# Kernel optimization log

Measured on AMD Instinct MI355X. Metric: run time of the kernel, lower is better.

Reference implementation:

```python
import jax, jax.numpy as jnp
import numpy as np
from jax import lax

LUT_SIZE = 33
BACKBONE_SIZE = 256
N_BASIS = 3


def _identity_lut(size):
    coords = jnp.linspace(0.0, 1.0, size)
    r, g, b = jnp.meshgrid(coords, coords, coords, indexing='ij')
    return jnp.stack([r.ravel(), g.ravel(), b.ravel()], axis=-1)  # [size^3, 3]


def setup_inputs() -> dict:
    key = jax.random.key(0)
    k_img, k_lut, k1, k2, kd = jax.random.split(key, 5)
    B, H, W = 4, 1080, 1920
    image = jax.random.uniform(k_img, (B, 3, H, W), dtype=jnp.float32)
    ident = _identity_lut(LUT_SIZE)  # [35937, 3]
    basis_luts = ident[None].repeat(N_BASIS, axis=0) + 0.05 * jax.random.normal(k_lut, (N_BASIS, LUT_SIZE ** 3, 3), dtype=jnp.float32)
    conv1_w = jax.random.normal(k1, (16, 3, 3, 3), dtype=jnp.float32) * 0.1
    conv1_b = jnp.zeros((16,), jnp.float32)
    conv2_w = jax.random.normal(k2, (32, 16, 3, 3), dtype=jnp.float32) * 0.1
    conv2_b = jnp.zeros((32,), jnp.float32)
    dense_w = jax.random.normal(kd, (32, 3), dtype=jnp.float32) * 0.1
    dense_b = jnp.zeros((3,), jnp.float32)
    return {"image": image, "basis_luts": basis_luts, "conv1_w": conv1_w, "conv1_b": conv1_b,
            "conv2_w": conv2_w, "conv2_b": conv2_b, "dense_w": dense_w, "dense_b": dense_b}


def _backbone(thumb, conv1_w, conv1_b, conv2_w, conv2_b, dense_w, dense_b):
    # Lightweight CNN -> softmax weights over basis LUTs. [B,3,256,256] -> [B,n_basis]
    x = lax.conv_general_dilated(thumb, conv1_w, (2, 2), 'SAME') + conv1_b[None, :, None, None]
    x = jax.nn.relu(x)
    x = lax.conv_general_dilated(x, conv2_w, (2, 2), 'SAME') + conv2_b[None, :, None, None]
    x = jax.nn.relu(x)
    x = x.mean(axis=(2, 3))  # global average pool -> [B, 32]
    return jax.nn.softmax(x @ dense_w + dense_b, axis=-1)


def _apply_lut(image, lut):
    # image [B,3,H,W] in [0,1]; lut [B,S,S,S,3] laid out as (r,g,b) grid axes.
    # Replicates F.grid_sample(mode='bilinear', padding_mode='border', align_corners=True)
    # on a 5D volume where grid x-coord = R channel -> LUT's b-axis (last grid axis),
    # y = G -> g-axis, z = B -> r-axis (exactly the axis mapping of the torch code).
    B, C, H, W = image.shape
    S = lut.shape[1]
    px = image.transpose(0, 2, 3, 1).reshape(B, H * W, 3)  # [B,P,3] = (R,G,B)
    pos = jnp.clip(px, 0.0, 1.0) * (S - 1)  # align_corners=True + border clamp
    i0 = jnp.clip(jnp.floor(pos).astype(jnp.int32), 0, S - 2)
    f = pos - i0.astype(pos.dtype)
    i1 = i0 + 1
    # axis mapping: z (LUT axis 0) <- channel 2 (Blue); y (axis 1) <- G; x (axis 2) <- R
    z0, y0, x0 = i0[..., 2], i0[..., 1], i0[..., 0]
    z1, y1, x1 = i1[..., 2], i1[..., 1], i1[..., 0]
    fz, fy, fx = f[..., 2], f[..., 1], f[..., 0]
    lut_flat = lut.reshape(B, S * S * S, 3)

    def gather(z, y, x):
        idx = (z * S + y) * S + x  # [B,P]
        return jnp.take_along_axis(lut_flat, idx[..., None], axis=1)  # [B,P,3]

    wz0, wz1 = (1.0 - fz)[..., None], fz[..., None]
    wy0, wy1 = (1.0 - fy)[..., None], fy[..., None]
    wx0, wx1 = (1.0 - fx)[..., None], fx[..., None]
    out = (wz0 * (wy0 * (wx0 * gather(z0, y0, x0) + wx1 * gather(z0, y0, x1))
                  + wy1 * (wx0 * gather(z0, y1, x0) + wx1 * gather(z0, y1, x1)))
           + wz1 * (wy0 * (wx0 * gather(z1, y0, x0) + wx1 * gather(z1, y0, x1))
                    + wy1 * (wx0 * gather(z1, y1, x0) + wx1 * gather(z1, y1, x1))))
    out = out.reshape(B, H, W, 3).transpose(0, 3, 1, 2)
    return jnp.clip(out, 0.0, 1.0)


def reference(image, basis_luts, conv1_w, conv1_b, conv2_w, conv2_b, dense_w, dense_b):
    B = image.shape[0]
    S = LUT_SIZE
    thumb = jax.image.resize(image, (B, 3, BACKBONE_SIZE, BACKBONE_SIZE), method='linear')
    weights = _backbone(thumb, conv1_w, conv1_b, conv2_w, conv2_b, dense_w, dense_b)  # [B,n]
    blended = jnp.einsum('bn,npc->bpc', weights, basis_luts)  # [B, S^3, 3]
    lut = blended.reshape(B, S, S, S, 3)
    return _apply_lut(image, lut)
```

## Files before the change

kernel.cpp:

```cpp
#include <hip/hip_runtime.h>
#include <hip/hip_bf16.h>
#include <hip/hip_fp16.h>

#define LUT_S 33
#define LUT_P (LUT_S*LUT_S*LUT_S)
#define CELLS 32768
#define IMG_H 1080
#define IMG_W 1920
#define TH 256
#define TW 256

__global__ __launch_bounds__(256)
void resize_w_kernel(const float* __restrict__ img, float* __restrict__ tmp) {
    __shared__ float srow[IMG_W];
    int r = blockIdx.x;
    const float4* row4 = (const float4*)(img + (size_t)r * IMG_W);
    float4* s4 = (float4*)srow;
    for (int i = threadIdx.x; i < IMG_W / 4; i += 256) s4[i] = row4[i];
    __syncthreads();
    int ow = threadIdx.x;
    const float kscale = 7.5f;
    float sf = (ow + 0.5f) * 7.5f - 0.5f;
    int lo = (int)ceilf(sf - kscale); if (lo < 0) lo = 0;
    int hi = (int)floorf(sf + kscale); if (hi > IMG_W - 1) hi = IMG_W - 1;
    float acc = 0.f, wsum = 0.f;
    for (int i = lo; i <= hi; ++i) {
        float w = 1.0f - fabsf(sf - (float)i) * (1.0f / 7.5f);
        if (w > 0.f) { acc += w * srow[i]; wsum += w; }
    }
    tmp[(size_t)r * TW + ow] = acc / wsum;
}

__global__ void resize_h_kernel(const float* __restrict__ tmp,
                                float* __restrict__ thumb, int total) {
    int e = blockIdx.x * blockDim.x + threadIdx.x;
    if (e >= total) return;
    int ow = e & 255;
    int oh = (e >> 8) & 255;
    int pl = e >> 16;
    const float kscale = 4.21875f;
    float sf = (oh + 0.5f) * 4.21875f - 0.5f;
    int lo = (int)ceilf(sf - kscale); if (lo < 0) lo = 0;
    int hi = (int)floorf(sf + kscale); if (hi > IMG_H - 1) hi = IMG_H - 1;
    const float* col = tmp + (size_t)pl * IMG_H * TW + ow;
    float acc = 0.f, wsum = 0.f;
    for (int i = lo; i <= hi; ++i) {
        float w = 1.0f - fabsf(sf - (float)i) * (1.0f / 4.21875f);
        if (w > 0.f) { acc += w * col[(size_t)i * TW]; wsum += w; }
    }
    thumb[e] = acc / wsum;
}

__global__ void conv1_kernel(const float* __restrict__ thumb,
                             const float* __restrict__ w,
                             const float* __restrict__ bias,
                             float* __restrict__ out, int total) {
    int e = blockIdx.x * blockDim.x + threadIdx.x;
    if (e >= total) return;
    int ow = e & 127;
    int oh = (e >> 7) & 127;
    int b  = e >> 14;
    float acc[16];
    #pragma unroll
    for (int oc = 0; oc < 16; ++oc) acc[oc] = bias[oc];
    for (int ic = 0; ic < 3; ++ic) {
        const float* tp = thumb + ((size_t)(b * 3 + ic) * 256) * 256;
        #pragma unroll
        for (int kh = 0; kh < 3; ++kh) {
            int ih = oh * 2 + kh;
            if (ih >= 256) continue;
            #pragma unroll
            for (int kw = 0; kw < 3; ++kw) {
                int iw = ow * 2 + kw;
                if (iw >= 256) continue;
                float v = tp[ih * 256 + iw];
                #pragma unroll
                for (int oc = 0; oc < 16; ++oc)
                    acc[oc] += v * w[(oc * 3 + ic) * 9 + kh * 3 + kw];
            }
        }
    }
    size_t o = ((size_t)b * 16 << 14) + (oh << 7) + ow;
    #pragma unroll
    for (int oc = 0; oc < 16; ++oc)
        out[o + ((size_t)oc << 14)] = fmaxf(acc[oc], 0.f);
}

__global__ void conv2_pool_kernel(const float* __restrict__ c1,
                                  const float* __restrict__ w,
                                  const float* __restrict__ bias,
                                  float* __restrict__ partial, int total) {
    int e = blockIdx.x * blockDim.x + threadIdx.x;
    if (e >= total) return;
    int sp = e & 4095;
    int g  = (e >> 12) & 3;
    int b  = e >> 14;
    int ow = sp & 63, oh = sp >> 6;
    float acc[8];
    #pragma unroll
    for (int j = 0; j < 8; ++j) acc[j] = bias[g * 8 + j];
    for (int ic = 0; ic < 16; ++ic) {
        const float* ip = c1 + ((size_t)(b * 16 + ic) << 14);
        #pragma unroll
        for (int kh = 0; kh < 3; ++kh) {
            int ih = oh * 2 + kh;
            if (ih >= 128) continue;
            #pragma unroll
            for (int kw = 0; kw < 3; ++kw) {
                int iw = ow * 2 + kw;
                if (iw >= 128) continue;
                float v = ip[(ih << 7) + iw];
                #pragma unroll
                for (int j = 0; j < 8; ++j)
                    acc[j] += v * w[((g * 8 + j) * 16 + ic) * 9 + kh * 3 + kw];
            }
        }
    }
    #pragma unroll
    for (int j = 0; j < 8; ++j) {
        float val = fmaxf(acc[j], 0.f);
        #pragma unroll
        for (int off = 32; off > 0; off >>= 1) val += __shfl_down(val, off, 64);
        acc[j] = val;
    }
    if ((threadIdx.x & 63) == 0) {
        #pragma unroll
        for (int j = 0; j < 8; ++j)
            partial[((b * 32 + g * 8 + j) << 6) + oh] = acc[j];
    }
}

__global__ void head_kernel(const float* __restrict__ partial,
                            const float* __restrict__ dw,
                            const float* __restrict__ db,
                            float* __restrict__ wts, int B) {
    __shared__ float sp[8 * 32];
    __shared__ float lg[8 * 3];
    int t = threadIdx.x;
    if (t < B * 32) {
        const float4* p4 = (const float4*)(partial + (t << 6));
        float s = 0.f;
        #pragma unroll
        for (int i = 0; i < 16; ++i) {
            float4 v = p4[i];
            s += v.x + v.y + v.z + v.w;
        }
        sp[t] = s * (1.0f / 4096.0f);
    }
    __syncthreads();
    if (t < B * 3) {
        int b = t / 3, n = t - b * 3;
        float acc = db[n];
        for (int ch = 0; ch < 32; ++ch) acc += sp[b * 32 + ch] * dw[ch * 3 + n];
        lg[t] = acc;
    }
    __syncthreads();
    if (t < B) {
        float a = lg[t * 3 + 0], bb = lg[t * 3 + 1], c = lg[t * 3 + 2];
        float m = fmaxf(a, fmaxf(bb, c));
        float e0 = expf(a - m), e1 = expf(bb - m), e2 = expf(c - m);
        float inv = 1.0f / (e0 + e1 + e2);
        wts[t * 3 + 0] = e0 * inv;
        wts[t * 3 + 1] = e1 * inv;
        wts[t * 3 + 2] = e2 * inv;
    }
}

__global__ void blend_cells_kernel(const float* __restrict__ basis,
                                   const float* __restrict__ wts,
                                   uint4* __restrict__ cells, int total) {
    int e = blockIdx.x * blockDim.x + threadIdx.x;
    if (e >= total) return;
    int b    = e >> 15;
    int cidx = e & (CELLS - 1);
    int cx = cidx & 31, cy = (cidx >> 5) & 31, cz = cidx >> 10;
    float w0 = wts[b * 3 + 0], w1 = wts[b * 3 + 1], w2 = wts[b * 3 + 2];
    const float* b0 = basis;
    const float* b1 = basis + (size_t)LUT_P * 3;
    const float* b2 = basis + (size_t)2 * LUT_P * 3;
    float v[24];
    float mn = 1e30f, mx = -1e30f;
    #pragma unroll
    for (int c = 0; c < 8; ++c) {
        int dx = c & 1, dy = (c >> 1) & 1, dz = c >> 2;
        size_t o = (size_t)(((cz + dz) * LUT_S + cy + dy) * LUT_S + cx + dx) * 3;
        #pragma unroll
        for (int ch = 0; ch < 3; ++ch) {
            float val = w0 * b0[o + ch] + w1 * b1[o + ch] + w2 * b2[o + ch];
            v[ch * 8 + c] = val;
            mn = fminf(mn, val); mx = fmaxf(mx, val);
        }
    }
    float range = mx - mn;
    float inv = (range > 1e-20f) ? 255.0f / range : 0.0f;
    float scale = range * (1.0f / 255.0f);
    unsigned int d[6];
    #pragma unroll
    for (int k = 0; k < 6; ++k) {
        unsigned int pk = 0;
        #pragma unroll
        for (int j = 0; j < 4; ++j) {
            float q = (v[k * 4 + j] - mn) * inv;
            int qi = (int)rintf(q);
            qi = qi < 0 ? 0 : (qi > 255 ? 255 : qi);
            pk |= ((unsigned int)qi) << (8 * j);
        }
        d[k] = pk;
    }
    uint4* outp = cells + ((size_t)e << 1);
    outp[0] = make_uint4(d[0], d[1], d[2], d[3]);
    outp[1] = make_uint4(d[4], d[5], __float_as_uint(scale), __float_as_uint(mn));
}

__device__ __forceinline__ float trilerp_u8(unsigned int lo, unsigned int hi,
                                            float fx, float fy, float fz) {
    float q000 = (float)(lo & 0xffu);
    float q100 = (float)((lo >> 8) & 0xffu);
    float q010 = (float)((lo >> 16) & 0xffu);
    float q110 = (float)((lo >> 24) & 0xffu);
    float q001 = (float)(hi & 0xffu);
    float q101 = (float)((hi >> 8) & 0xffu);
    float q011 = (float)((hi >> 16) & 0xffu);
    float q111 = (float)((hi >> 24) & 0xffu);
    float a0 = q000 + fx * (q100 - q000);
    float a1 = q010 + fx * (q110 - q010);
    float b0 = q001 + fx * (q101 - q001);
    float b1 = q011 + fx * (q111 - q011);
    float c0 = a0 + fy * (a1 - a0);
    float c1 = b0 + fy * (b1 - b0);
    return c0 + fz * (c1 - c0);
}

__global__ __launch_bounds__(256)
void apply_lut_kernel(const float* __restrict__ img,
                      const uint4* __restrict__ cells,
                      float* __restrict__ out, int total_quads) {
    const int P  = IMG_H * IMG_W;
    const int QP = P / 4;
    int t = blockIdx.x * blockDim.x + threadIdx.x;
    if (t >= total_quads) return;
    int b = t / QP;
    int q = t - b * QP;
    const uint4* cbase = cells + ((size_t)b * CELLS << 1);
    size_t base = (size_t)b * 3 * P + (size_t)q * 4;
    float4 R  = *(const float4*)(img + base);
    float4 G  = *(const float4*)(img + base + P);
    float4 Bl = *(const float4*)(img + base + 2 * (size_t)P);
    float4 Ro, Go, Bo;
    float* rp = (float*)&R; float* gp = (float*)&G; float* bp = (float*)&Bl;
    float* rop = (float*)&Ro; float* gop = (float*)&Go; float* bop = (float*)&Bo;
    #pragma unroll
    for (int k = 0; k < 4; ++k) {
        float pr = fminf(fmaxf(rp[k], 0.f), 1.f) * (float)(LUT_S - 1);
        float pg = fminf(fmaxf(gp[k], 0.f), 1.f) * (float)(LUT_S - 1);
        float pb = fminf(fmaxf(bp[k], 0.f), 1.f) * (float)(LUT_S - 1);
        int ix = (int)pr; if (ix > LUT_S - 2) ix = LUT_S - 2;
        int iy = (int)pg; if (iy > LUT_S - 2) iy = LUT_S - 2;
        int iz = (int)pb; if (iz > LUT_S - 2) iz = LUT_S - 2;
        float fx = pr - (float)ix, fy = pg - (float)iy, fz = pb - (float)iz;
        int cidx = (iz << 10) | (iy << 5) | ix;
        const uint4* cp = cbase + ((size_t)cidx << 1);
        uint4 A  = cp[0];
        uint4 Bq = cp[1];
        float scale = __uint_as_float(Bq.z);
        float offs  = __uint_as_float(Bq.w);
        float tr = trilerp_u8(A.x, A.y, fx, fy, fz);
        float tg = trilerp_u8(A.z, A.w, fx, fy, fz);
        float tb = trilerp_u8(Bq.x, Bq.y, fx, fy, fz);
        rop[k] = fminf(fmaxf(tr * scale + offs, 0.f), 1.f);
        gop[k] = fminf(fmaxf(tg * scale + offs, 0.f), 1.f);
        bop[k] = fminf(fmaxf(tb * scale + offs, 0.f), 1.f);
    }
    *(float4*)(out + base)                 = Ro;
    *(float4*)(out + base + P)             = Go;
    *(float4*)(out + base + 2 * (size_t)P) = Bo;
}

extern "C" void kernel_launch(void* const* d_in, const int* in_sizes, int n_in,
                              void* d_out, int out_size, void* d_ws, size_t ws_size,
                              hipStream_t stream) {
    const float* img     = (const float*)d_in[0];
    const float* basis   = (const float*)d_in[1];
    const float* conv1_w = (const float*)d_in[2];
    const float* conv1_b = (const float*)d_in[3];
    const float* conv2_w = (const float*)d_in[4];
    const float* conv2_b = (const float*)d_in[5];
    const float* dense_w = (const float*)d_in[6];
    const float* dense_b = (const float*)d_in[7];
    float* out = (float*)d_out;

    const size_t P = (size_t)IMG_H * IMG_W;
    int B = (int)(in_sizes[0] / (3 * P));

    float* ws = (float*)d_ws;
    size_t off = 0;
    float* tmp1    = ws + off; off += (size_t)B * 3 * IMG_H * TW;
    float* thumb   = ws + off; off += (size_t)B * 3 * TH * TW;
    float* c1      = ws + off; off += (size_t)B * 16 * 128 * 128;
    float* partial = ws + off; off += (size_t)B * 32 * 64;
    float* wts     = ws + off; off += (size_t)B * 3;
    off = (off + 3) & ~(size_t)3;
    uint4* cells   = (uint4*)(ws + off); off += (size_t)B * CELLS * 8;

    const int TPB = 256;
    {
        resize_w_kernel<<<B * 3 * IMG_H, TPB, 0, stream>>>(img, tmp1);
    }
    {
        int total = B * 3 * TH * TW;
        resize_h_kernel<<<(total + TPB - 1) / TPB, TPB, 0, stream>>>(tmp1, thumb, total);
    }
    {
        int total = B * 128 * 128;
        conv1_kernel<<<(total + TPB - 1) / TPB, TPB, 0, stream>>>(thumb, conv1_w, conv1_b, c1, total);
    }
    {
        int total = B * 4 * 4096;
        conv2_pool_kernel<<<(total + TPB - 1) / TPB, TPB, 0, stream>>>(c1, conv2_w, conv2_b, partial, total);
    }
    {
        head_kernel<<<1, TPB, 0, stream>>>(partial, dense_w, dense_b, wts, B);
    }
    {
        int total = B * CELLS;
        blend_cells_kernel<<<(total + TPB - 1) / TPB, TPB, 0, stream>>>(basis, wts, cells, total);
    }
    {
        int total = B * (int)(P / 4);
        apply_lut_kernel<<<(total + TPB - 1) / TPB, TPB, 0, stream>>>(img, cells, out, total);
    }
}
```

Before: 295.3 us.

## Split conv channel groups across more threads and batch LUT gathers with nontemporal stores

conv1 now has each thread compute 4 output channels instead of 16, and conv2 computes 2 instead of 8. This launches 4x and 8x more threads to raise occupancy and parallelism in the small backbone convs, at the cost of more redundant input loads. In the LUT apply kernel, all four pixels' cell gathers are issued before any interpolation, so their memory latency overlaps. Outputs are written with nontemporal stores to avoid polluting the cache.

```diff
diff --git a/kernel.cpp b/kernel.cpp
--- a/kernel.cpp
+++ b/kernel.cpp
@@ -9,6 +9,8 @@
 #define IMG_W 1920
 #define TH 256
 #define TW 256
+
+typedef float f4 __attribute__((ext_vector_type(4)));
 
 __global__ __launch_bounds__(256)
 void resize_w_kernel(const float* __restrict__ img, float* __restrict__ tmp) {
@@ -59,12 +61,13 @@
     if (e >= total) return;
     int ow = e & 127;
     int oh = (e >> 7) & 127;
-    int b  = e >> 14;
-    float acc[16];
-    #pragma unroll
-    for (int oc = 0; oc < 16; ++oc) acc[oc] = bias[oc];
+    int g  = (e >> 14) & 3;
+    int b  = e >> 16;
+    float acc[4];
+    #pragma unroll
+    for (int j = 0; j < 4; ++j) acc[j] = bias[g * 4 + j];
     for (int ic = 0; ic < 3; ++ic) {
-        const float* tp = thumb + ((size_t)(b * 3 + ic) * 256) * 256;
+        const float* tp = thumb + ((size_t)(b * 3 + ic) << 16);
         #pragma unroll
         for (int kh = 0; kh < 3; ++kh) {
             int ih = oh * 2 + kh;
@@ -73,17 +76,17 @@
             for (int kw = 0; kw < 3; ++kw) {
                 int iw = ow * 2 + kw;
                 if (iw >= 256) continue;
-                float v = tp[ih * 256 + iw];
+                float v = tp[(ih << 8) + iw];
                 #pragma unroll
-                for (int oc = 0; oc < 16; ++oc)
-                    acc[oc] += v * w[(oc * 3 + ic) * 9 + kh * 3 + kw];
+                for (int j = 0; j < 4; ++j)
+                    acc[j] += v * w[((g * 4 + j) * 3 + ic) * 9 + kh * 3 + kw];
             }
         }
     }
-    size_t o = ((size_t)b * 16 << 14) + (oh << 7) + ow;
-    #pragma unroll
-    for (int oc = 0; oc < 16; ++oc)
-        out[o + ((size_t)oc << 14)] = fmaxf(acc[oc], 0.f);
+    size_t o = ((size_t)(b * 16 + g * 4) << 14) + (oh << 7) + ow;
+    #pragma unroll
+    for (int j = 0; j < 4; ++j)
+        out[o + ((size_t)j << 14)] = fmaxf(acc[j], 0.f);
 }
 
 __global__ void conv2_pool_kernel(const float* __restrict__ c1,
@@ -93,12 +96,12 @@
     int e = blockIdx.x * blockDim.x + threadIdx.x;
     if (e >= total) return;
     int sp = e & 4095;
-    int g  = (e >> 12) & 3;
-    int b  = e >> 14;
+    int g  = (e >> 12) & 15;
+    int b  = e >> 16;
     int ow = sp & 63, oh = sp >> 6;
-    float acc[8];
-    #pragma unroll
-    for (int j = 0; j < 8; ++j) acc[j] = bias[g * 8 + j];
+    float acc[2];
+    #pragma unroll
+    for (int j = 0; j < 2; ++j) acc[j] = bias[g * 2 + j];
     for (int ic = 0; ic < 16; ++ic) {
         const float* ip = c1 + ((size_t)(b * 16 + ic) << 14);
         #pragma unroll
@@ -111,13 +114,13 @@
                 if (iw >= 128) continue;
                 float v = ip[(ih << 7) + iw];
                 #pragma unroll
-                for (int j = 0; j < 8; ++j)
-                    acc[j] += v * w[((g * 8 + j) * 16 + ic) * 9 + kh * 3 + kw];
+                for (int j = 0; j < 2; ++j)
+                    acc[j] += v * w[((g * 2 + j) * 16 + ic) * 9 + kh * 3 + kw];
             }
         }
     }
     #pragma unroll
-    for (int j = 0; j < 8; ++j) {
+    for (int j = 0; j < 2; ++j) {
         float val = fmaxf(acc[j], 0.f);
         #pragma unroll
         for (int off = 32; off > 0; off >>= 1) val += __shfl_down(val, off, 64);
@@ -125,8 +128,8 @@
     }
     if ((threadIdx.x & 63) == 0) {
         #pragma unroll
-        for (int j = 0; j < 8; ++j)
-            partial[((b * 32 + g * 8 + j) << 6) + oh] = acc[j];
+        for (int j = 0; j < 2; ++j)
+            partial[((b * 32 + g * 2 + j) << 6) + oh] = acc[j];
     }
 }
 
@@ -243,37 +246,46 @@
     int q = t - b * QP;
     const uint4* cbase = cells + ((size_t)b * CELLS << 1);
     size_t base = (size_t)b * 3 * P + (size_t)q * 4;
-    float4 R  = *(const float4*)(img + base);
-    float4 G  = *(const float4*)(img + base + P);
-    float4 Bl = *(const float4*)(img + base + 2 * (size_t)P);
-    float4 Ro, Go, Bo;
-    float* rp = (float*)&R; float* gp = (float*)&G; float* bp = (float*)&Bl;
-    float* rop = (float*)&Ro; float* gop = (float*)&Go; float* bop = (float*)&Bo;
+    f4 R  = *(const f4*)(img + base);
+    f4 G  = *(const f4*)(img + base + P);
+    f4 Bl = *(const f4*)(img + base + 2 * (size_t)P);
+
+    int cidx[4]; float fx[4], fy[4], fz[4];
     #pragma unroll
     for (int k = 0; k < 4; ++k) {
-        float pr = fminf(fmaxf(rp[k], 0.f), 1.f) * (float)(LUT_S - 1);
-        float pg = fminf(fmaxf(gp[k], 0.f), 1.f) * (float)(LUT_S - 1);
-        float pb = fminf(fmaxf(bp[k], 0.f), 1.f) * (float)(LUT_S - 1);
+        float pr = fminf(fmaxf(R[k], 0.f), 1.f) * (float)(LUT_S - 1);
+        float pg = fminf(fmaxf(G[k], 0.f), 1.f) * (float)(LUT_S - 1);
+        float pb = fminf(fmaxf(Bl[k], 0.f), 1.f) * (float)(LUT_S - 1);
         int ix = (int)pr; if (ix > LUT_S - 2) ix = LUT_S - 2;
         int iy = (int)pg; if (iy > LUT_S - 2) iy = LUT_S - 2;
         int iz = (int)pb; if (iz > LUT_S - 2) iz = LUT_S - 2;
-        float fx = pr - (float)ix, fy = pg - (float)iy, fz = pb - (float)iz;
-        int cidx = (iz << 10) | (iy << 5) | ix;
-        const uint4* cp = cbase + ((size_t)cidx << 1);
-        uint4 A  = cp[0];
-        uint4 Bq = cp[1];
-        float scale = __uint_as_float(Bq.z);
-        float offs  = __uint_as_float(Bq.w);
-        float tr = trilerp_u8(A.x, A.y, fx, fy, fz);
-        float tg = trilerp_u8(A.z, A.w, fx, fy, fz);
-        float tb = trilerp_u8(Bq.x, Bq.y, fx, fy, fz);
-        rop[k] = fminf(fmaxf(tr * scale + offs, 0.f), 1.f);
-        gop[k] = fminf(fmaxf(tg * scale + offs, 0.f), 1.f);
-        bop[k] = fminf(fmaxf(tb * scale + offs, 0.f), 1.f);
-    }
-    *(float4*)(out + base)                 = Ro;
-    *(float4*)(out + base + P)             = Go;
-    *(float4*)(out + base + 2 * (size_t)P) = Bo;
+        fx[k] = pr - (float)ix;
+        fy[k] = pg - (float)iy;
+        fz[k] = pb - (float)iz;
+        cidx[k] = (iz << 10) | (iy << 5) | ix;
+    }
+    uint4 A[4], Bq[4];
+    #pragma unroll
+    for (int k = 0; k < 4; ++k) {
+        const uint4* cp = cbase + ((size_t)cidx[k] << 1);
+        A[k]  = cp[0];
+        Bq[k] = cp[1];
+    }
+    f4 Ro, Go, Bo;
+    #pragma unroll
+    for (int k = 0; k < 4; ++k) {
+        float scale = __uint_as_float(Bq[k].z);
+        float offs  = __uint_as_float(Bq[k].w);
+        float tr = trilerp_u8(A[k].x, A[k].y, fx[k], fy[k], fz[k]);
+        float tg = trilerp_u8(A[k].z, A[k].w, fx[k], fy[k], fz[k]);
+        float tb = trilerp_u8(Bq[k].x, Bq[k].y, fx[k], fy[k], fz[k]);
+        Ro[k] = fminf(fmaxf(tr * scale + offs, 0.f), 1.f);
+        Go[k] = fminf(fmaxf(tg * scale + offs, 0.f), 1.f);
+        Bo[k] = fminf(fmaxf(tb * scale + offs, 0.f), 1.f);
+    }
+    __builtin_nontemporal_store(Ro, (f4*)(out + base));
+    __builtin_nontemporal_store(Go, (f4*)(out + base + P));
+    __builtin_nontemporal_store(Bo, (f4*)(out + base + 2 * (size_t)P));
 }
 
 extern "C" void kernel_launch(void* const* d_in, const int* in_sizes, int n_in,
@@ -311,11 +323,11 @@
         resize_h_kernel<<<(total + TPB - 1) / TPB, TPB, 0, stream>>>(tmp1, thumb, total);
     }
     {
-        int total = B * 128 * 128;
+        int total = B * 4 * 128 * 128;
         conv1_kernel<<<(total + TPB - 1) / TPB, TPB, 0, stream>>>(thumb, conv1_w, conv1_b, c1, total);
     }
     {
-        int total = B * 4 * 4096;
+        int total = B * 16 * 4096;
         conv2_pool_kernel<<<(total + TPB - 1) / TPB, TPB, 0, stream>>>(c1, conv2_w, conv2_b, partial, total);
     }
     {
```

Measured after the change: 289.2 us. -2.1%, faster.
